# Optimization experiments

Hardware: AMD Instinct MI355X
Metric: run time of the kernel (lower is better)

Reference implementation:

```python
import jax, jax.numpy as jnp
import numpy as np

B, T, D_IN = 8192, 12, 64   # trajectories, traj length (== max_length), input dim
HID, ENC, R = 512, 128, 64  # encoder hidden, encoded_dim, MPS rank
OUT = 1


def _uniform(key, shape, bound):
    return jax.random.uniform(key, shape, jnp.float32, -bound, bound)


def setup_inputs() -> dict:
    key = jax.random.key(0)
    ks = jax.random.split(key, 8)
    x = jax.random.normal(ks[0], (B, T, D_IN), jnp.float32)
    # encoder Linear params (Kaiming-uniform-like scale)
    W1 = _uniform(ks[1], (HID, D_IN), 1.0 / np.sqrt(D_IN))
    b1 = _uniform(ks[2], (HID,), 1.0 / np.sqrt(D_IN))
    W2 = _uniform(ks[3], (ENC, HID), 1.0 / np.sqrt(HID))
    b2 = _uniform(ks[4], (ENC,), 1.0 / np.sqrt(HID))
    # MPS cores with if_rescale_weights bound = 1/sqrt(prod(dims))
    H_first = _uniform(ks[5], (1, ENC, R), 1.0 / np.sqrt(1 * ENC * R))
    H_mid = _uniform(ks[6], (T - 2, R, ENC, R), 1.0 / np.sqrt(R * ENC * R))
    H_last = _uniform(ks[7], (R, ENC, OUT), 1.0 / np.sqrt(R * ENC * OUT))
    return {"x": x, "W1": W1, "b1": b1, "W2": W2, "b2": b2,
            "H_first": H_first, "H_mid": H_mid, "H_last": H_last}


def reference(x, W1, b1, W2, b2, H_first, H_mid, H_last):
    Bn, Tn, _ = x.shape
    # two-layer encoder MLP with ReLU after each layer
    h = jax.nn.relu(jnp.einsum('btd,hd->bth', x, W1) + b1)
    enc = jax.nn.relu(jnp.einsum('bth,eh->bte', h, W2) + b2)  # [B, T, ENC]
    # contract each timestep's encoding with its core along the physical dim
    v = jnp.einsum('be,oer->br', enc[:, 0], H_first)              # [B, R] (dim0==1 squeezed)
    M = jnp.einsum('bte,tper->btpr', enc[:, 1:Tn - 1], H_mid)     # [B, T-2, R, R]
    # sequential chain product (vector-matrix, associative scan structure)
    for t in range(Tn - 2):
        v = jnp.einsum('bp,bpr->br', v, M[:, t])
    last = jnp.einsum('be,per->bpr', enc[:, -1], H_last)          # [B, R, OUT]
    out = jnp.einsum('bp,bpo->bo', v, last)                       # [B, OUT]
    return out.squeeze(-1)                                        # [B] (output_dim == 1)
```

## Files before the change

### kernel.cpp

```cpp
#include <hip/hip_runtime.h>
#include <hip/hip_fp16.h>


#define B_ALL 8192
#define TT    12
#define B_T   32
#define NBLK  256

typedef short bfrag __attribute__((ext_vector_type(8)));
typedef _Float16 hfrag __attribute__((ext_vector_type(8)));
typedef float ffrag __attribute__((ext_vector_type(16)));

#define O_ENC   0ULL
#define O_HMH   25165824ULL
#define O_HML   35651584ULL
#define O_W1F   46137344ULL
#define O_W2F   46202880ULL

__device__ __forceinline__ unsigned short bf16_rne(float f) {
    unsigned int u = __builtin_bit_cast(unsigned int, f);
    unsigned int r = (u + 0x7fffu + ((u >> 16) & 1u)) >> 16;
    return (unsigned short)r;
}
__device__ __forceinline__ float bf16_f32(unsigned short h) {
    unsigned int u = ((unsigned int)h) << 16;
    return __builtin_bit_cast(float, u);
}

__global__ __launch_bounds__(256)
void prep_kernel(const float* __restrict__ W1, const float* __restrict__ W2,
                 const float* __restrict__ Hm,
                 __half* __restrict__ w1f, __half* __restrict__ w2f,
                 unsigned short* __restrict__ Hh, unsigned short* __restrict__ Hl)
{
    const int tid = threadIdx.x;
    const int bid = blockIdx.x;
    if (bid < 1280) {
        __shared__ unsigned short hs[4096], ls[4096];
        const int t = bid >> 7, e = bid & 127;
        const float* src = Hm + ((size_t)t * 64 * 128 + e) * 64;
        const int p  = tid >> 2;
        const int rc = (tid & 3) * 16;
        const int fp = (p >> 4) * 512 + ((p >> 3) & 1) * 256 + (p & 7);
        #pragma unroll
        for (int k4 = 0; k4 < 4; ++k4) {
            const int r0 = rc + k4 * 4;
            const float4 v4 = *(const float4*)&src[(size_t)p * 8192 + r0];
            const float vv[4] = {v4.x, v4.y, v4.z, v4.w};
            #pragma unroll
            for (int k = 0; k < 4; ++k) {
                const int r = r0 + k;
                const int f = (r >> 5) * 2048 + (r & 31) * 8 + fp;
                const float val = vv[k];
                const unsigned short hi = bf16_rne(val);
                const unsigned short lo = bf16_rne(val - bf16_f32(hi));
                hs[f] = hi;
                ls[f] = lo;
            }
        }
        __syncthreads();
        const size_t q0 = (size_t)t * 524288 + (size_t)e * 4096 + tid * 16;
        *(uint4*)&Hh[q0]     = *(const uint4*)&hs[tid * 16];
        *(uint4*)&Hh[q0 + 8] = *(const uint4*)&hs[tid * 16 + 8];
        *(uint4*)&Hl[q0]     = *(const uint4*)&ls[tid * 16];
        *(uint4*)&Hl[q0 + 8] = *(const uint4*)&ls[tid * 16 + 8];
    } else {
        const int wb = bid - 1280;
        const long long N_W1 = 32768, N_W2 = 65536;
        for (long long idx = wb * 256 + tid; idx < N_W1 + N_W2; idx += 8 * 256) {
            if (idx < N_W1) {
                const int w = (int)idx;
                const int jn = w >> 11, ks = (w >> 9) & 3, half = (w >> 8) & 1;
                const int jl = (w >> 3) & 31, jj = w & 7;
                const int j = jn * 32 + jl, d = ks * 16 + half * 8 + jj;
                w1f[w] = __float2half(W1[j * 64 + d]);
            } else {
                const int w = (int)(idx - N_W1);
                const int en = w >> 14, ks2g = (w >> 9) & 31, half = (w >> 8) & 1;
                const int el = (w >> 3) & 31, jj = w & 7;
                const int e = en * 32 + el, j = ks2g * 16 + half * 8 + jj;
                w2f[w] = __float2half(W2[e * 512 + j]);
            }
        }
    }
}

__global__ __launch_bounds__(256)
void enc_kernel(const float* __restrict__ x,
                const float* __restrict__ b1, const float* __restrict__ b2,
                const __half* __restrict__ w1f, const __half* __restrict__ w2f,
                __half* __restrict__ encH)
{
    __shared__ __align__(16) unsigned char smem[17408];
    float* x_s  = (float*)smem;
    __half* h_s = (__half*)smem;

    const int tid   = threadIdx.x;
    const int wv    = tid >> 6;
    const int lane  = tid & 63;
    const int l32   = lane & 31;
    const int half  = lane >> 5;
    const int msub  = wv >> 1;
    const int nhalf = wv & 1;
    const int m0    = blockIdx.x * 64;

    #pragma unroll
    for (int i = 0; i < 4; ++i) {
        const int f4 = i * 256 + tid;
        const int r = f4 >> 4, c4 = (f4 & 15) * 4;
        *(float4*)&x_s[r * 68 + c4] =
            *(const float4*)&x[(long long)(m0 + r) * 64 + c4];
    }
    __syncthreads();

    hfrag xa[4];
    #pragma unroll
    for (int ks = 0; ks < 4; ++ks) {
        const float* src = &x_s[(msub * 32 + l32) * 68 + ks * 16 + half * 8];
        const float4 a = *(const float4*)src;
        const float4 b = *(const float4*)(src + 4);
        hfrag v;
        v[0] = (_Float16)a.x; v[1] = (_Float16)a.y;
        v[2] = (_Float16)a.z; v[3] = (_Float16)a.w;
        v[4] = (_Float16)b.x; v[5] = (_Float16)b.y;
        v[6] = (_Float16)b.z; v[7] = (_Float16)b.w;
        xa[ks] = v;
    }
    __syncthreads();

    ffrag c2[2];
    c2[0] = 0.0f; c2[1] = 0.0f;

    for (int chunk = 0; chunk < 4; ++chunk) {
        ffrag c1[2];
        float b1j[2];
        #pragma unroll
        for (int nf = 0; nf < 2; ++nf) {
            const int jn = chunk * 4 + nhalf * 2 + nf;
            b1j[nf] = b1[jn * 32 + l32];
            ffrag acc = 0.0f;
            #pragma unroll
            for (int ks = 0; ks < 4; ++ks) {
                const hfrag bh = *(const hfrag*)(w1f + (jn * 4 + ks) * 512
                                                 + half * 256 + l32 * 8);
                acc = __builtin_amdgcn_mfma_f32_32x32x16_f16(xa[ks], bh, acc, 0, 0, 0);
            }
            c1[nf] = acc;
        }
        __syncthreads();
        #pragma unroll
        for (int nf = 0; nf < 2; ++nf) {
            #pragma unroll
            for (int i2 = 0; i2 < 16; ++i2) {
                const int m_row = (i2 & 3) + 8 * (i2 >> 2) + 4 * half;
                const float v = fmaxf(c1[nf][i2] + b1j[nf], 0.0f);
                h_s[(msub * 32 + m_row) * 136 + nhalf * 64 + nf * 32 + l32] =
                    __float2half(v);
            }
        }
        __syncthreads();
        #pragma unroll
        for (int ks2 = 0; ks2 < 8; ++ks2) {
            const hfrag a = *(const hfrag*)&h_s[(msub * 32 + l32) * 136
                                                + ks2 * 16 + half * 8];
            const int ks2g = chunk * 8 + ks2;
            #pragma unroll
            for (int ef = 0; ef < 2; ++ef) {
                const int en = nhalf * 2 + ef;
                const hfrag b = *(const hfrag*)(w2f + (en * 32 + ks2g) * 512
                                                + half * 256 + l32 * 8);
                c2[ef] = __builtin_amdgcn_mfma_f32_32x32x16_f16(a, b, c2[ef], 0, 0, 0);
            }
        }
    }

    #pragma unroll
    for (int ef = 0; ef < 2; ++ef) {
        const int e = nhalf * 64 + ef * 32 + l32;
        const float b2e = b2[e];
        #pragma unroll
        for (int i2 = 0; i2 < 16; ++i2) {
            const int m_row = (i2 & 3) + 8 * (i2 >> 2) + 4 * half;
            const int m_g = m0 + msub * 32 + m_row;
            encH[(long long)m_g * 128 + e] =
                __float2half(fmaxf(c2[ef][i2] + b2e, 0.0f));
        }
    }
}

__global__ __launch_bounds__(512, 1)
void chain_all(const unsigned short* __restrict__ HmH,
               const unsigned short* __restrict__ HmL,
               const __half* __restrict__ encH,
               const float* __restrict__ Hf,
               const float* __restrict__ HL,
               float* __restrict__ out)
{
    __shared__ __align__(16) unsigned char smem[60480];
    float* vsum  = (float*)smem;
    float* enc_s = (float*)(smem + 8448);
    float* scr   = (float*)(smem + 25344);
    float* hl_s  = (float*)(smem + 25344);
    float* red   = (float*)(smem + 58368);

    const int tid  = threadIdx.x;
    const int b0   = blockIdx.x * B_T;
    const int lane = tid & 63;
    const int wv   = tid >> 6;
    const int l32  = lane & 31;
    const int half = lane >> 5;
    const int eq   = wv >> 1;
    const int rh   = wv & 1;

    const int sbL = tid >> 4;
    const int seo = (tid & 15) * 8;
    #define STAGE_ENC(T)                                                      \
    {                                                                         \
        const __half* er_ = encH + ((size_t)(b0 + sbL) * 12 + (T)) * 128 + seo;\
        uint4 u = *(const uint4*)er_;                                         \
        const __half* hp_ = (const __half*)&u;                                \
        _Pragma("unroll")                                                     \
        for (int j = 0; j < 8; ++j)                                           \
            enc_s[(seo + j) * 33 + sbL] = __half2float(hp_[j]);               \
    }

    {
        STAGE_ENC(0);
        __syncthreads();
        const int bI = tid & 31, pg = tid >> 5;
        const int p0 = pg * 4;
        float a0 = 0, a1 = 0, a2 = 0, a3 = 0;
        for (int e = 0; e < 128; ++e) {
            const float ev = enc_s[e * 33 + bI];
            const float4 h = *(const float4*)&Hf[e * 64 + p0];
            a0 += ev * h.x; a1 += ev * h.y; a2 += ev * h.z; a3 += ev * h.w;
        }
        vsum[(p0 + 0) * 33 + bI] = a0;
        vsum[(p0 + 1) * 33 + bI] = a1;
        vsum[(p0 + 2) * 33 + bI] = a2;
        vsum[(p0 + 3) * 33 + bI] = a3;
        __syncthreads();
    }

    const unsigned short* Hsh = HmH;
    const unsigned short* Hsl = HmL;
    const int lanoff = rh * 2048 + half * 256 + l32 * 8;

    #pragma unroll 1
    for (int t = 1; t <= 10; ++t) {
        STAGE_ENC(t);

        bfrag vbh[4], vbl[4];
        #pragma unroll
        for (int s = 0; s < 4; ++s) {
            const int p0 = s * 16 + half * 8;
            bfrag hb, lb;
            #pragma unroll
            for (int j = 0; j < 8; ++j) {
                const float f = vsum[(p0 + j) * 33 + l32];
                const unsigned short hi = bf16_rne(f);
                const unsigned short lo = bf16_rne(f - bf16_f32(hi));
                hb[j] = (short)hi;
                lb[j] = (short)lo;
            }
            vbh[s] = hb;
            vbl[s] = lb;
        }
        __syncthreads();

        const unsigned short* hp = Hsh + (size_t)(eq * 32) * 4096 + lanoff;
        const unsigned short* lp = Hsl + (size_t)(eq * 32) * 4096 + lanoff;
        bfrag cah[4], cal[4];
        #pragma unroll
        for (int s = 0; s < 4; ++s) {
            cah[s] = *(const bfrag*)(hp + s * 512);
            cal[s] = *(const bfrag*)(lp + s * 512);
        }
        ffrag z = 0.0f;
        ffrag vn = 0.0f;
        #pragma unroll 2
        for (int e = 0; e < 32; ++e) {
            hp += 4096; lp += 4096;
            bfrag nah[4], nal[4];
            #pragma unroll
            for (int s = 0; s < 4; ++s) {
                nah[s] = *(const bfrag*)(hp + s * 512);
                nal[s] = *(const bfrag*)(lp + s * 512);
            }
            const float ev = enc_s[(eq * 32 + e) * 33 + l32];
            ffrag w = z;
            #pragma unroll
            for (int s = 0; s < 4; ++s) {
                w = __builtin_amdgcn_mfma_f32_32x32x16_bf16(cah[s], vbh[s], w, 0, 0, 0);
                w = __builtin_amdgcn_mfma_f32_32x32x16_bf16(cah[s], vbl[s], w, 0, 0, 0);
                w = __builtin_amdgcn_mfma_f32_32x32x16_bf16(cal[s], vbh[s], w, 0, 0, 0);
            }
            vn += w * ev;
            #pragma unroll
            for (int s = 0; s < 4; ++s) { cah[s] = nah[s]; cal[s] = nal[s]; }
        }
        __syncthreads();

        float4* sc4 = (float4*)scr;
        if (eq != 0) {
            const int slot = (eq - 1) * 2 + rh;
            #pragma unroll
            for (int q = 0; q < 4; ++q) {
                float4 f4 = {vn[q * 4 + 0], vn[q * 4 + 1],
                             vn[q * 4 + 2], vn[q * 4 + 3]};
                sc4[(slot * 4 + q) * 66 + lane] = f4;
            }
        }
        __syncthreads();
        if (eq == 0) {
            #pragma unroll
            for (int g = 1; g < 4; ++g) {
                const int slot = (g - 1) * 2 + rh;
                #pragma unroll
                for (int q = 0; q < 4; ++q) {
                    const float4 f4 = sc4[(slot * 4 + q) * 66 + lane];
                    vn[q * 4 + 0] += f4.x; vn[q * 4 + 1] += f4.y;
                    vn[q * 4 + 2] += f4.z; vn[q * 4 + 3] += f4.w;
                }
            }
            #pragma unroll
            for (int i = 0; i < 16; ++i) {
                const int r = rh * 32 + (i & 3) + 8 * (i >> 2) + 4 * half;
                vsum[r * 33 + l32] = vn[i];
            }
        }
        __syncthreads();

        Hsh += 524288;
        Hsl += 524288;
    }

    {
        STAGE_ENC(11);
        #pragma unroll
        for (int i = 0; i < 16; ++i) {
            const int idx = i * 512 + tid;
            hl_s[(idx >> 7) * 129 + (idx & 127)] = HL[idx];
        }
        __syncthreads();
        const int bI = tid & 31, pg = tid >> 5;
        const int p0 = pg * 4;
        float s = 0.0f;
        #pragma unroll
        for (int i = 0; i < 4; ++i) {
            float L = 0.0f;
            #pragma unroll 16
            for (int e = 0; e < 128; ++e)
                L += enc_s[e * 33 + bI] * hl_s[(p0 + i) * 129 + e];
            s += vsum[(p0 + i) * 33 + bI] * L;
        }
        red[pg * 33 + bI] = s;
        __syncthreads();
        if (tid < 32) {
            float acc = 0.0f;
            #pragma unroll
            for (int g = 0; g < 16; ++g)
                acc += red[g * 33 + tid];
            out[b0 + tid] = acc;
        }
    }
    #undef STAGE_ENC
}

extern "C" void kernel_launch(void* const* d_in, const int* in_sizes, int n_in,
                              void* d_out, int out_size, void* d_ws, size_t ws_size,
                              hipStream_t stream) {
    const float* x  = (const float*)d_in[0];
    const float* W1 = (const float*)d_in[1];
    const float* b1 = (const float*)d_in[2];
    const float* W2 = (const float*)d_in[3];
    const float* b2 = (const float*)d_in[4];
    const float* Hf = (const float*)d_in[5];
    const float* Hm = (const float*)d_in[6];
    const float* HL = (const float*)d_in[7];
    float* out = (float*)d_out;
    (void)in_sizes; (void)n_in; (void)out_size; (void)ws_size;

    char* ws = (char*)d_ws;
    __half* encH        = (__half*)(ws + O_ENC);
    unsigned short* HmH = (unsigned short*)(ws + O_HMH);
    unsigned short* HmL = (unsigned short*)(ws + O_HML);
    __half* w1f         = (__half*)(ws + O_W1F);
    __half* w2f         = (__half*)(ws + O_W2F);

    prep_kernel<<<dim3(1288), dim3(256), 0, stream>>>(W1, W2, Hm, w1f, w2f, HmH, HmL);
    enc_kernel<<<dim3(1536), dim3(256), 0, stream>>>(x, b1, b2, w1f, w2f, encH);
    chain_all<<<dim3(NBLK), dim3(512), 0, stream>>>(HmH, HmL, encH, Hf, HL, out);
}
```

Baseline: 414.9 us.

## Fuse encoder MLP into chain kernel with register-resident weights

Removes the separate encoder kernel and computes the two-layer MLP inside chain_all for each block's 32 trajectories, looping over the 12 timesteps. W1 and W2 fragments are held in registers per wave, and the encoded result is written back to the workspace for the chain stage. This saves one kernel launch and the weight refetches, but only 256 blocks of 512 threads now do the encoder work, half the waves sit idle during layer 2, there are four barriers per timestep, and the large register footprint (32 W2 fragments) may cause spills.

```diff
diff --git a/kernel.cpp b/kernel.cpp
--- a/kernel.cpp
+++ b/kernel.cpp
@@ -85,113 +85,13 @@
     }
 }
 
-__global__ __launch_bounds__(256)
-void enc_kernel(const float* __restrict__ x,
-                const float* __restrict__ b1, const float* __restrict__ b2,
-                const __half* __restrict__ w1f, const __half* __restrict__ w2f,
-                __half* __restrict__ encH)
-{
-    __shared__ __align__(16) unsigned char smem[17408];
-    float* x_s  = (float*)smem;
-    __half* h_s = (__half*)smem;
-
-    const int tid   = threadIdx.x;
-    const int wv    = tid >> 6;
-    const int lane  = tid & 63;
-    const int l32   = lane & 31;
-    const int half  = lane >> 5;
-    const int msub  = wv >> 1;
-    const int nhalf = wv & 1;
-    const int m0    = blockIdx.x * 64;
-
-    #pragma unroll
-    for (int i = 0; i < 4; ++i) {
-        const int f4 = i * 256 + tid;
-        const int r = f4 >> 4, c4 = (f4 & 15) * 4;
-        *(float4*)&x_s[r * 68 + c4] =
-            *(const float4*)&x[(long long)(m0 + r) * 64 + c4];
-    }
-    __syncthreads();
-
-    hfrag xa[4];
-    #pragma unroll
-    for (int ks = 0; ks < 4; ++ks) {
-        const float* src = &x_s[(msub * 32 + l32) * 68 + ks * 16 + half * 8];
-        const float4 a = *(const float4*)src;
-        const float4 b = *(const float4*)(src + 4);
-        hfrag v;
-        v[0] = (_Float16)a.x; v[1] = (_Float16)a.y;
-        v[2] = (_Float16)a.z; v[3] = (_Float16)a.w;
-        v[4] = (_Float16)b.x; v[5] = (_Float16)b.y;
-        v[6] = (_Float16)b.z; v[7] = (_Float16)b.w;
-        xa[ks] = v;
-    }
-    __syncthreads();
-
-    ffrag c2[2];
-    c2[0] = 0.0f; c2[1] = 0.0f;
-
-    for (int chunk = 0; chunk < 4; ++chunk) {
-        ffrag c1[2];
-        float b1j[2];
-        #pragma unroll
-        for (int nf = 0; nf < 2; ++nf) {
-            const int jn = chunk * 4 + nhalf * 2 + nf;
-            b1j[nf] = b1[jn * 32 + l32];
-            ffrag acc = 0.0f;
-            #pragma unroll
-            for (int ks = 0; ks < 4; ++ks) {
-                const hfrag bh = *(const hfrag*)(w1f + (jn * 4 + ks) * 512
-                                                 + half * 256 + l32 * 8);
-                acc = __builtin_amdgcn_mfma_f32_32x32x16_f16(xa[ks], bh, acc, 0, 0, 0);
-            }
-            c1[nf] = acc;
-        }
-        __syncthreads();
-        #pragma unroll
-        for (int nf = 0; nf < 2; ++nf) {
-            #pragma unroll
-            for (int i2 = 0; i2 < 16; ++i2) {
-                const int m_row = (i2 & 3) + 8 * (i2 >> 2) + 4 * half;
-                const float v = fmaxf(c1[nf][i2] + b1j[nf], 0.0f);
-                h_s[(msub * 32 + m_row) * 136 + nhalf * 64 + nf * 32 + l32] =
-                    __float2half(v);
-            }
-        }
-        __syncthreads();
-        #pragma unroll
-        for (int ks2 = 0; ks2 < 8; ++ks2) {
-            const hfrag a = *(const hfrag*)&h_s[(msub * 32 + l32) * 136
-                                                + ks2 * 16 + half * 8];
-            const int ks2g = chunk * 8 + ks2;
-            #pragma unroll
-            for (int ef = 0; ef < 2; ++ef) {
-                const int en = nhalf * 2 + ef;
-                const hfrag b = *(const hfrag*)(w2f + (en * 32 + ks2g) * 512
-                                                + half * 256 + l32 * 8);
-                c2[ef] = __builtin_amdgcn_mfma_f32_32x32x16_f16(a, b, c2[ef], 0, 0, 0);
-            }
-        }
-    }
-
-    #pragma unroll
-    for (int ef = 0; ef < 2; ++ef) {
-        const int e = nhalf * 64 + ef * 32 + l32;
-        const float b2e = b2[e];
-        #pragma unroll
-        for (int i2 = 0; i2 < 16; ++i2) {
-            const int m_row = (i2 & 3) + 8 * (i2 >> 2) + 4 * half;
-            const int m_g = m0 + msub * 32 + m_row;
-            encH[(long long)m_g * 128 + e] =
-                __float2half(fmaxf(c2[ef][i2] + b2e, 0.0f));
-        }
-    }
-}
-
 __global__ __launch_bounds__(512, 1)
 void chain_all(const unsigned short* __restrict__ HmH,
                const unsigned short* __restrict__ HmL,
-               const __half* __restrict__ encH,
+               const float* __restrict__ x,
+               const float* __restrict__ b1, const float* __restrict__ b2,
+               const __half* __restrict__ w1f, const __half* __restrict__ w2f,
+               __half* __restrict__ encH,
                const float* __restrict__ Hf,
                const float* __restrict__ HL,
                float* __restrict__ out)
@@ -202,6 +102,9 @@
     float* scr   = (float*)(smem + 25344);
     float* hl_s  = (float*)(smem + 25344);
     float* red   = (float*)(smem + 58368);
+    float*  x_s     = (float*)smem;
+    __half* h_s     = (__half*)(smem + 8704);
+    float*  enc_tmp = (float*)(smem + 41600);
 
     const int tid  = threadIdx.x;
     const int b0   = blockIdx.x * B_T;
@@ -211,6 +114,93 @@
     const int half = lane >> 5;
     const int eq   = wv >> 1;
     const int rh   = wv & 1;
+
+    {
+        const int jn0 = wv * 2;
+        hfrag w1a[2][4];
+        float b1j[2];
+        #pragma unroll
+        for (int nf = 0; nf < 2; ++nf) {
+            b1j[nf] = b1[(jn0 + nf) * 32 + l32];
+            #pragma unroll
+            for (int ks = 0; ks < 4; ++ks)
+                w1a[nf][ks] = *(const hfrag*)(w1f + ((jn0 + nf) * 4 + ks) * 512
+                                              + half * 256 + l32 * 8);
+        }
+        const int en = wv;
+        hfrag w2b[32];
+        float b2v = 0.0f;
+        if (wv < 4) {
+            b2v = b2[en * 32 + l32];
+            #pragma unroll
+            for (int k2 = 0; k2 < 32; ++k2)
+                w2b[k2] = *(const hfrag*)(w2f + (en * 32 + k2) * 512
+                                          + half * 256 + l32 * 8);
+        }
+
+        #pragma unroll 1
+        for (int t = 0; t < TT; ++t) {
+            {
+                const int row = tid >> 4, c4 = (tid & 15) * 4;
+                *(float4*)&x_s[row * 68 + c4] =
+                    *(const float4*)&x[((size_t)(b0 + row) * 12 + t) * 64 + c4];
+            }
+            __syncthreads();
+            hfrag xa[4];
+            #pragma unroll
+            for (int ks = 0; ks < 4; ++ks) {
+                const float* src = &x_s[l32 * 68 + ks * 16 + half * 8];
+                const float4 a = *(const float4*)src;
+                const float4 b = *(const float4*)(src + 4);
+                hfrag v;
+                v[0] = (_Float16)a.x; v[1] = (_Float16)a.y;
+                v[2] = (_Float16)a.z; v[3] = (_Float16)a.w;
+                v[4] = (_Float16)b.x; v[5] = (_Float16)b.y;
+                v[6] = (_Float16)b.z; v[7] = (_Float16)b.w;
+                xa[ks] = v;
+            }
+            #pragma unroll
+            for (int nf = 0; nf < 2; ++nf) {
+                ffrag acc = 0.0f;
+                #pragma unroll
+                for (int ks = 0; ks < 4; ++ks)
+                    acc = __builtin_amdgcn_mfma_f32_32x32x16_f16(xa[ks], w1a[nf][ks],
+                                                                 acc, 0, 0, 0);
+                #pragma unroll
+                for (int i2 = 0; i2 < 16; ++i2) {
+                    const int m_row = (i2 & 3) + 8 * (i2 >> 2) + 4 * half;
+                    const float v = fmaxf(acc[i2] + b1j[nf], 0.0f);
+                    h_s[m_row * 514 + (jn0 + nf) * 32 + l32] = __float2half(v);
+                }
+            }
+            __syncthreads();
+            if (wv < 4) {
+                ffrag c2 = 0.0f;
+                #pragma unroll
+                for (int k2 = 0; k2 < 32; ++k2) {
+                    const hfrag a = *(const hfrag*)&h_s[l32 * 514 + k2 * 16 + half * 8];
+                    c2 = __builtin_amdgcn_mfma_f32_32x32x16_f16(a, w2b[k2], c2, 0, 0, 0);
+                }
+                #pragma unroll
+                for (int i2 = 0; i2 < 16; ++i2) {
+                    const int m_row = (i2 & 3) + 8 * (i2 >> 2) + 4 * half;
+                    enc_tmp[(en * 32 + l32) * 33 + m_row] =
+                        fmaxf(c2[i2] + b2v, 0.0f);
+                }
+            }
+            __syncthreads();
+            {
+                const int bl = tid >> 4, eo = (tid & 15) * 8;
+                __half hv[8];
+                #pragma unroll
+                for (int j = 0; j < 8; ++j)
+                    hv[j] = __float2half(enc_tmp[(eo + j) * 33 + bl]);
+                *(uint4*)&encH[((size_t)(b0 + bl) * 12 + t) * 128 + eo] =
+                    *(const uint4*)hv;
+            }
+            __syncthreads();
+        }
+    }
 
     const int sbL = tid >> 4;
     const int seo = (tid & 15) * 8;
@@ -389,6 +379,6 @@
     __half* w2f         = (__half*)(ws + O_W2F);
 
     prep_kernel<<<dim3(1288), dim3(256), 0, stream>>>(W1, W2, Hm, w1f, w2f, HmH, HmL);
-    enc_kernel<<<dim3(1536), dim3(256), 0, stream>>>(x, b1, b2, w1f, w2f, encH);
-    chain_all<<<dim3(NBLK), dim3(512), 0, stream>>>(HmH, HmL, encH, Hf, HL, out);
-}
+    chain_all<<<dim3(NBLK), dim3(512), 0, stream>>>(HmH, HmL, x, b1, b2, w1f, w2f,
+                                                    encH, Hf, HL, out);
+}
```

Result: slower. 440.7 us (+6.2%).

## Split weight prep and fold H-core conversion into encoder launch

Applied to the files above, without the earlier changes.

The small W1/W2 fp16 conversion moves into its own short kernel. The larger H_mid bf16 hi/lo split conversion now runs as extra blocks of the encoder kernel, so it overlaps with encoder compute instead of running as a serialized launch before it. This removes one dependency stage from the critical path, but the encoder grid becomes larger and its blocks carry mixed shared-memory and register needs.

```diff
diff --git a/kernel.cpp b/kernel.cpp
--- a/kernel.cpp
+++ b/kernel.cpp
@@ -28,16 +28,42 @@
 }
 
 __global__ __launch_bounds__(256)
-void prep_kernel(const float* __restrict__ W1, const float* __restrict__ W2,
-                 const float* __restrict__ Hm,
-                 __half* __restrict__ w1f, __half* __restrict__ w2f,
-                 unsigned short* __restrict__ Hh, unsigned short* __restrict__ Hl)
+void prep_w(const float* __restrict__ W1, const float* __restrict__ W2,
+            __half* __restrict__ w1f, __half* __restrict__ w2f)
 {
+    const int idx = blockIdx.x * 256 + threadIdx.x;
+    if (idx < 32768) {
+        const int w = idx;
+        const int jn = w >> 11, ks = (w >> 9) & 3, half = (w >> 8) & 1;
+        const int jl = (w >> 3) & 31, jj = w & 7;
+        const int j = jn * 32 + jl, d = ks * 16 + half * 8 + jj;
+        w1f[w] = __float2half(W1[j * 64 + d]);
+    } else {
+        const int w = idx - 32768;
+        const int en = w >> 14, ks2g = (w >> 9) & 31, half = (w >> 8) & 1;
+        const int el = (w >> 3) & 31, jj = w & 7;
+        const int e = en * 32 + el, j = ks2g * 16 + half * 8 + jj;
+        w2f[w] = __float2half(W2[e * 512 + j]);
+    }
+}
+
+__global__ __launch_bounds__(256)
+void enc_conv(const float* __restrict__ x,
+              const float* __restrict__ b1, const float* __restrict__ b2,
+              const __half* __restrict__ w1f, const __half* __restrict__ w2f,
+              __half* __restrict__ encH,
+              const float* __restrict__ Hm,
+              unsigned short* __restrict__ Hh, unsigned short* __restrict__ Hl)
+{
+    __shared__ __align__(16) unsigned char smem[17408];
     const int tid = threadIdx.x;
     const int bid = blockIdx.x;
-    if (bid < 1280) {
-        __shared__ unsigned short hs[4096], ls[4096];
-        const int t = bid >> 7, e = bid & 127;
+
+    if (bid >= 1536) {
+        unsigned short* hs = (unsigned short*)smem;
+        unsigned short* ls = (unsigned short*)(smem + 8192);
+        const int hb = bid - 1536;
+        const int t = hb >> 7, e = hb & 127;
         const float* src = Hm + ((size_t)t * 64 * 128 + e) * 64;
         const int p  = tid >> 2;
         const int rc = (tid & 3) * 16;
@@ -64,45 +90,19 @@
         *(uint4*)&Hh[q0 + 8] = *(const uint4*)&hs[tid * 16 + 8];
         *(uint4*)&Hl[q0]     = *(const uint4*)&ls[tid * 16];
         *(uint4*)&Hl[q0 + 8] = *(const uint4*)&ls[tid * 16 + 8];
-    } else {
-        const int wb = bid - 1280;
-        const long long N_W1 = 32768, N_W2 = 65536;
-        for (long long idx = wb * 256 + tid; idx < N_W1 + N_W2; idx += 8 * 256) {
-            if (idx < N_W1) {
-                const int w = (int)idx;
-                const int jn = w >> 11, ks = (w >> 9) & 3, half = (w >> 8) & 1;
-                const int jl = (w >> 3) & 31, jj = w & 7;
-                const int j = jn * 32 + jl, d = ks * 16 + half * 8 + jj;
-                w1f[w] = __float2half(W1[j * 64 + d]);
-            } else {
-                const int w = (int)(idx - N_W1);
-                const int en = w >> 14, ks2g = (w >> 9) & 31, half = (w >> 8) & 1;
-                const int el = (w >> 3) & 31, jj = w & 7;
-                const int e = en * 32 + el, j = ks2g * 16 + half * 8 + jj;
-                w2f[w] = __float2half(W2[e * 512 + j]);
-            }
-        }
-    }
-}
-
-__global__ __launch_bounds__(256)
-void enc_kernel(const float* __restrict__ x,
-                const float* __restrict__ b1, const float* __restrict__ b2,
-                const __half* __restrict__ w1f, const __half* __restrict__ w2f,
-                __half* __restrict__ encH)
-{
-    __shared__ __align__(16) unsigned char smem[17408];
+        return;
+    }
+
     float* x_s  = (float*)smem;
     __half* h_s = (__half*)smem;
 
-    const int tid   = threadIdx.x;
     const int wv    = tid >> 6;
     const int lane  = tid & 63;
     const int l32   = lane & 31;
     const int half  = lane >> 5;
     const int msub  = wv >> 1;
     const int nhalf = wv & 1;
-    const int m0    = blockIdx.x * 64;
+    const int m0    = bid * 64;
 
     #pragma unroll
     for (int i = 0; i < 4; ++i) {
@@ -388,7 +388,8 @@
     __half* w1f         = (__half*)(ws + O_W1F);
     __half* w2f         = (__half*)(ws + O_W2F);
 
-    prep_kernel<<<dim3(1288), dim3(256), 0, stream>>>(W1, W2, Hm, w1f, w2f, HmH, HmL);
-    enc_kernel<<<dim3(1536), dim3(256), 0, stream>>>(x, b1, b2, w1f, w2f, encH);
+    prep_w<<<dim3(384), dim3(256), 0, stream>>>(W1, W2, w1f, w2f);
+    enc_conv<<<dim3(2816), dim3(256), 0, stream>>>(x, b1, b2, w1f, w2f, encH,
+                                                   Hm, HmH, HmL);
     chain_all<<<dim3(NBLK), dim3(512), 0, stream>>>(HmH, HmL, encH, Hf, HL, out);
 }
```

After: 408.2 us. About the same (-1.6%).
